# Optimization experiments

Hardware: AMD Instinct MI355X
Metric: run time of the kernel (lower is better)

The kernel has to match this reference:

```python
import jax, jax.numpy as jnp
import numpy as np

GROUP_SIZE = 256
QMIN_W, QMAX_W = -8, 7  # int4
QMIN_A, QMAX_A = -128, 127  # int8


def per_token_fake_quant(x):
    """torchao choose_qparams_per_token_asymmetric + quant + dequant (int8)."""
    mn = jnp.minimum(jnp.min(x, axis=-1, keepdims=True), 0.0)
    mx = jnp.maximum(jnp.max(x, axis=-1, keepdims=True), 0.0)
    eps = jnp.finfo(jnp.float32).eps
    scale = jnp.maximum((mx - mn) / float(QMAX_A - QMIN_A), eps)
    dmin = mn / scale
    dmax = mx / scale
    zp = jnp.where((QMIN_A + dmin) + (QMAX_A + dmax) > 0, QMIN_A - dmin, QMAX_A - dmax)
    zp = jnp.round(jnp.clip(zp, QMIN_A, QMAX_A))
    q = jnp.clip(jnp.round(x / scale) + zp, QMIN_A, QMAX_A)
    return (q - zp) * scale


def setup_inputs() -> dict:
    key = jax.random.key(0)
    k1, k2, k3, k4 = jax.random.split(key, 4)
    T, O, I = 8192, 4096, 4096
    x = jax.random.normal(k1, (T, I), dtype=jnp.float32)
    weight = jax.random.randint(k2, (O, I), QMIN_W, QMAX_W + 1, dtype=jnp.int32)
    scales = jax.random.uniform(k3, (O, I // GROUP_SIZE), dtype=jnp.float32,
                                minval=0.005, maxval=0.02)
    zeros = jnp.round(jax.random.uniform(k4, (O, I // GROUP_SIZE), dtype=jnp.float32,
                                         minval=-4.0, maxval=4.0))
    return {"x": x, "weight": weight, "scales": scales, "zeros": zeros}


def reference(x, weight, scales, zeros):
    # dynamic per-token int8 fake-quant of the activation
    x_dq = per_token_fake_quant(x.astype(jnp.float32))
    # groupwise int4 weight dequant: (w - zero) * scale per group
    O, I = weight.shape
    w = weight.astype(jnp.float32).reshape(O, I // GROUP_SIZE, GROUP_SIZE)
    w_dq = ((w - zeros[..., None]) * scales[..., None]).reshape(O, I)
    # linear: [T, I] @ [I, O] -> [T, O]
    return jnp.einsum('ti,oi->to', x_dq, w_dq)
```

## Files before the change

kernel.cpp:

```cpp
#include <hip/hip_runtime.h>
#include <hip/hip_bf16.h>
#include <math.h>

typedef __attribute__((ext_vector_type(8))) __bf16 bf16x8;
typedef __attribute__((ext_vector_type(4))) float f32x4;

#define BM 256
#define BN 256
#define BK 64

__device__ __forceinline__ void glds16(const void* g, void* l) {
  __builtin_amdgcn_global_load_lds(
      (const __attribute__((address_space(1))) void*)g,
      (__attribute__((address_space(3))) void*)l, 16, 0, 0);
}

__device__ __forceinline__ unsigned short f2bf(float f) {
  __hip_bfloat16 h = __float2bfloat16(f);
  return __builtin_bit_cast(unsigned short, h);
}

__global__ __launch_bounds__(256) void prep_x(const float* __restrict__ x,
                                              ushort* __restrict__ xq,
                                              int I) {
  const int wave = threadIdx.x >> 6, lane = threadIdx.x & 63;
  const int row = blockIdx.x * 4 + wave;
  const float4* xr = (const float4*)(x + (size_t)row * I);
  float4 v[16];
#pragma unroll
  for (int j = 0; j < 16; ++j) v[j] = xr[lane + j * 64];
  float mn = 0.f, mx = 0.f;
#pragma unroll
  for (int j = 0; j < 16; ++j) {
    mn = fminf(mn, fminf(fminf(v[j].x, v[j].y), fminf(v[j].z, v[j].w)));
    mx = fmaxf(mx, fmaxf(fmaxf(v[j].x, v[j].y), fmaxf(v[j].z, v[j].w)));
  }
#pragma unroll
  for (int off = 32; off > 0; off >>= 1) {
    mn = fminf(mn, __shfl_xor(mn, off));
    mx = fmaxf(mx, __shfl_xor(mx, off));
  }
  const float scale = fmaxf((mx - mn) / 255.0f, 1.1920928955078125e-07f);
  const float dmin = mn / scale, dmax = mx / scale;
  float zp = ((-128.0f + dmin) + (127.0f + dmax) > 0.0f) ? (-128.0f - dmin)
                                                         : (127.0f - dmax);
  zp = rintf(fminf(fmaxf(zp, -128.0f), 127.0f));
  const float rs = 1.0f / scale;
  ushort4* xo = (ushort4*)(xq + (size_t)row * I);
#pragma unroll
  for (int j = 0; j < 16; ++j) {
    ushort4 o;
    float q;
    q = fminf(fmaxf(rintf(v[j].x * rs) + zp, -128.f), 127.f);
    o.x = f2bf((q - zp) * scale);
    q = fminf(fmaxf(rintf(v[j].y * rs) + zp, -128.f), 127.f);
    o.y = f2bf((q - zp) * scale);
    q = fminf(fmaxf(rintf(v[j].z * rs) + zp, -128.f), 127.f);
    o.z = f2bf((q - zp) * scale);
    q = fminf(fmaxf(rintf(v[j].w * rs) + zp, -128.f), 127.f);
    o.w = f2bf((q - zp) * scale);
    xo[lane + j * 64] = o;
  }
}

__global__ __launch_bounds__(256) void prep_w(const int* __restrict__ w,
                                              const float* __restrict__ scales,
                                              const float* __restrict__ zeros,
                                              ushort* __restrict__ wq) {
  const long long base = (long long)blockIdx.x * 2048 + threadIdx.x;
  const int4* wr = (const int4*)w;
  ushort4* wo = (ushort4*)wq;
  int4 wv[8];
#pragma unroll
  for (int it = 0; it < 8; ++it) wv[it] = wr[base + (size_t)it * 256];
#pragma unroll
  for (int it = 0; it < 8; ++it) {
    const long long c = base + (size_t)it * 256;
    const int g = __builtin_amdgcn_readfirstlane((int)(c >> 6));
    const float s = scales[g];
    const float z = zeros[g];
    ushort4 ov;
    ov.x = f2bf(((float)wv[it].x - z) * s);
    ov.y = f2bf(((float)wv[it].y - z) * s);
    ov.z = f2bf(((float)wv[it].z - z) * s);
    ov.w = f2bf(((float)wv[it].w - z) * s);
    wo[c] = ov;
  }
}

__global__ __launch_bounds__(512, 2) void gemm_bt256(
    const ushort* __restrict__ A, const ushort* __restrict__ B,
    float* __restrict__ C, int M, int N, int K) {
  __shared__ __align__(16) ushort As[2][BM * BK];
  __shared__ __align__(16) ushort Bs[2][BN * BK];
  const int tid = threadIdx.x;
  const int wave = tid >> 6, lane = tid & 63;
  const int wm = wave >> 2;
  const int wn = wave & 3;

  const int nwg = gridDim.x;
  const int bid = blockIdx.x;
  const int swz =
      ((nwg & 7) == 0) ? ((bid & 7) * (nwg >> 3) + (bid >> 3)) : bid;
  const int ntn = N / BN;
  const int by = swz / ntn, bx = swz % ntn;
  const int bm0 = by * BM, bn0 = bx * BN;

  const int ldr = lane >> 3;
  const int ldc = ((lane & 7) ^ ldr) * 8;
  const ushort* Ag = A + (size_t)(bm0 + wave * 16 + ldr) * K + ldc;
  const ushort* Bg = B + (size_t)(bn0 + wave * 16 + ldr) * K + ldc;

#define STAGE_A(b, h, kt)                                        \
  do {                                                           \
    glds16(Ag + (size_t)((h) * 128) * K + (size_t)(kt) * BK,     \
           &As[b][((h) * 128 + wave * 16) * BK]);                \
    glds16(Ag + (size_t)((h) * 128 + 8) * K + (size_t)(kt) * BK, \
           &As[b][((h) * 128 + wave * 16 + 8) * BK]);            \
  } while (0)
#define STAGE_B(b, h, kt)                                        \
  do {                                                           \
    glds16(Bg + (size_t)((h) * 128) * K + (size_t)(kt) * BK,     \
           &Bs[b][((h) * 128 + wave * 16) * BK]);                \
    glds16(Bg + (size_t)((h) * 128 + 8) * K + (size_t)(kt) * BK, \
           &Bs[b][((h) * 128 + wave * 16 + 8) * BK]);            \
  } while (0)

  const int mrow = lane & 15;
  const int kc = lane >> 4;
  const int sw = mrow & 7;
  const int c0 = (kc ^ sw) * 8;
  const int c1 = ((4 + kc) ^ sw) * 8;
  const int aBase = (wm * 128 + mrow) * BK;
  const int bBase = (wn * 64 + mrow) * BK;

  f32x4 acc[8][4];
#pragma unroll
  for (int i = 0; i < 8; ++i)
#pragma unroll
    for (int j = 0; j < 4; ++j) acc[i][j] = (f32x4){0.f, 0.f, 0.f, 0.f};

  const int NT = K / BK;

  STAGE_A(0, 0, 0);
  STAGE_A(0, 1, 0);
  STAGE_B(0, 0, 0);
  STAGE_B(0, 1, 0);
  STAGE_B(1, 0, 1);
  STAGE_B(1, 1, 1);
  asm volatile("s_waitcnt vmcnt(4)" ::: "memory");
  __builtin_amdgcn_sched_barrier(0);
  __builtin_amdgcn_s_barrier();

  bf16x8 a[4][2], b[4][2];

#define MFMA8(MI0, NI0)                                                    \
  __builtin_amdgcn_s_setprio(1);                                           \
  _Pragma("unroll") for (int ks = 0; ks < 2; ++ks)                         \
      _Pragma("unroll") for (int mi = 0; mi < 4; ++mi)                     \
          _Pragma("unroll") for (int ni = 0; ni < 2; ++ni) acc[(MI0) + mi] \
              [(NI0) + ni] = __builtin_amdgcn_mfma_f32_16x16x32_bf16(      \
                  a[mi][ks], b[(NI0) + ni][ks], acc[(MI0) + mi][(NI0) + ni], \
                  0, 0, 0);                                                \
  __builtin_amdgcn_s_setprio(0);

#define KTILE(CUR, KT, DO_SA, DO_SB, WAIT4)                          \
  do {                                                               \
    const ushort* Ac = As[CUR];                                      \
    const ushort* Bc = Bs[CUR];                                      \
                             \
    _Pragma("unroll") for (int mi = 0; mi < 4; ++mi) {               \
      a[mi][0] = *(const bf16x8*)&Ac[aBase + mi * (16 * BK) + c0];   \
      a[mi][1] = *(const bf16x8*)&Ac[aBase + mi * (16 * BK) + c1];   \
    }                                                                \
    _Pragma("unroll") for (int ni = 0; ni < 2; ++ni) {               \
      b[ni][0] = *(const bf16x8*)&Bc[bBase + ni * (16 * BK) + c0];   \
      b[ni][1] = *(const bf16x8*)&Bc[bBase + ni * (16 * BK) + c1];   \
    }                                                                \
    if (DO_SA) STAGE_A(1 - (CUR), 0, (KT) + 1);                      \
    __builtin_amdgcn_s_barrier();                                    \
    MFMA8(0, 0)                                                      \
    __builtin_amdgcn_s_barrier();                                    \
                             \
    _Pragma("unroll") for (int ni = 2; ni < 4; ++ni) {               \
      b[ni][0] = *(const bf16x8*)&Bc[bBase + ni * (16 * BK) + c0];   \
      b[ni][1] = *(const bf16x8*)&Bc[bBase + ni * (16 * BK) + c1];   \
    }                                                                \
    if (DO_SA) STAGE_A(1 - (CUR), 1, (KT) + 1);                      \
    __builtin_amdgcn_s_barrier();                                    \
    MFMA8(0, 2)                                                      \
    __builtin_amdgcn_s_barrier();                                    \
                             \
    _Pragma("unroll") for (int mi = 0; mi < 4; ++mi) {               \
      a[mi][0] =                                                     \
          *(const bf16x8*)&Ac[aBase + (mi + 4) * (16 * BK) + c0];    \
      a[mi][1] =                                                     \
          *(const bf16x8*)&Ac[aBase + (mi + 4) * (16 * BK) + c1];    \
    }                                                                \
    if (DO_SB) STAGE_B(CUR, 0, (KT) + 2);                            \
    __builtin_amdgcn_s_barrier();                                    \
    MFMA8(4, 2)                                                      \
    __builtin_amdgcn_s_barrier();                                    \
                             \
    if (DO_SB) STAGE_B(CUR, 1, (KT) + 2);                            \
    if (WAIT4)                                                       \
      asm volatile("s_waitcnt vmcnt(4)" ::: "memory");               \
    else                                                             \
      asm volatile("s_waitcnt vmcnt(0)" ::: "memory");               \
    __builtin_amdgcn_sched_barrier(0);                               \
    __builtin_amdgcn_s_barrier();                                    \
    MFMA8(4, 0)                                                      \
    __builtin_amdgcn_s_barrier();                                    \
  } while (0)

  int kt = 0;
  for (; kt < NT - 2; kt += 2) {
    KTILE(0, kt, 1, 1, 1);
    KTILE(1, kt + 1, 1, 1, 1);
  }
  KTILE(0, kt, 1, 0, 0);
  KTILE(1, kt + 1, 0, 0, 0);

  const int col = lane & 15;
  const int rq = (lane >> 4) * 4;
#pragma unroll
  for (int mi = 0; mi < 8; ++mi)
#pragma unroll
    for (int ni = 0; ni < 4; ++ni) {
      const int r0 = bm0 + wm * 128 + mi * 16 + rq;
      const int c = bn0 + wn * 64 + ni * 16 + col;
#pragma unroll
      for (int r = 0; r < 4; ++r)
        C[(size_t)(r0 + r) * N + c] = acc[mi][ni][r];
    }
#undef KTILE
#undef MFMA8
#undef STAGE_A
#undef STAGE_B
}

extern "C" void kernel_launch(void* const* d_in, const int* in_sizes, int n_in,
                              void* d_out, int out_size, void* d_ws,
                              size_t ws_size, hipStream_t stream) {
  const float* x = (const float*)d_in[0];
  const int* w = (const int*)d_in[1];
  const float* scales = (const float*)d_in[2];
  const float* zeros = (const float*)d_in[3];
  float* out = (float*)d_out;

  const double ii =
      sqrt((double)in_sizes[0] * (double)in_sizes[1] / (double)out_size);
  const int I = (int)(ii + 0.5);
  const int T = in_sizes[0] / I;
  const int O = in_sizes[1] / I;

  ushort* xq = (ushort*)d_ws;
  ushort* wq = xq + (size_t)T * I;

  prep_x<<<T / 4, 256, 0, stream>>>(x, xq, I);
  prep_w<<<(int)(((long long)O * I) >> 13), 256, 0, stream>>>(w, scales,
                                                              zeros, wq);
  gemm_bt256<<<(O / BN) * (T / BM), 512, 0, stream>>>(xq, wq, out, T, O, I);
}
```

Before: 506.9 us.

## Replace bf16 GEMM with int8 MFMA and fold group scales and zero points

Activations and weights are now stored as exact int8 values: the per-token quantized x, and the weight with its group zero subtracted. The GEMM uses i32 int8 MFMA over 128-byte K tiles and applies each tile's per-group weight scale to the integer partial sums in fp32. The activation zero point is removed in the epilogue using a precomputed per-output-row sum U of scaled weights, plus the per-token scale and zero. This halves operand bytes and uses the higher-rate int8 matrix path, but adds VALU work converting and scaling integer partials on every K tile, and more LDS for the scale table.

```diff
diff --git a/kernel.cpp b/kernel.cpp
--- a/kernel.cpp
+++ b/kernel.cpp
@@ -2,12 +2,12 @@
 #include <hip/hip_bf16.h>
 #include <math.h>
 
-typedef __attribute__((ext_vector_type(8))) __bf16 bf16x8;
+typedef __attribute__((ext_vector_type(4))) int i32x4;
 typedef __attribute__((ext_vector_type(4))) float f32x4;
 
 #define BM 256
 #define BN 256
-#define BK 64
+#define BKB 128
 
 __device__ __forceinline__ void glds16(const void* g, void* l) {
   __builtin_amdgcn_global_load_lds(
@@ -15,13 +15,10 @@
       (__attribute__((address_space(3))) void*)l, 16, 0, 0);
 }
 
-__device__ __forceinline__ unsigned short f2bf(float f) {
-  __hip_bfloat16 h = __float2bfloat16(f);
-  return __builtin_bit_cast(unsigned short, h);
-}
-
 __global__ __launch_bounds__(256) void prep_x(const float* __restrict__ x,
-                                              ushort* __restrict__ xq,
+                                              char* __restrict__ xq,
+                                              float* __restrict__ sct,
+                                              float* __restrict__ zpt,
                                               int I) {
   const int wave = threadIdx.x >> 6, lane = threadIdx.x & 63;
   const int row = blockIdx.x * 4 + wave;
@@ -46,30 +43,33 @@
                                                          : (127.0f - dmax);
   zp = rintf(fminf(fmaxf(zp, -128.0f), 127.0f));
   const float rs = 1.0f / scale;
-  ushort4* xo = (ushort4*)(xq + (size_t)row * I);
+  if (lane == 0) {
+    sct[row] = scale;
+    zpt[row] = zp;
+  }
+  int* xo = (int*)(xq + (size_t)row * I);
 #pragma unroll
   for (int j = 0; j < 16; ++j) {
-    ushort4 o;
-    float q;
-    q = fminf(fmaxf(rintf(v[j].x * rs) + zp, -128.f), 127.f);
-    o.x = f2bf((q - zp) * scale);
-    q = fminf(fmaxf(rintf(v[j].y * rs) + zp, -128.f), 127.f);
-    o.y = f2bf((q - zp) * scale);
-    q = fminf(fmaxf(rintf(v[j].z * rs) + zp, -128.f), 127.f);
-    o.z = f2bf((q - zp) * scale);
-    q = fminf(fmaxf(rintf(v[j].w * rs) + zp, -128.f), 127.f);
-    o.w = f2bf((q - zp) * scale);
-    xo[lane + j * 64] = o;
+    const float q0 = fminf(fmaxf(rintf(v[j].x * rs) + zp, -128.f), 127.f);
+    const float q1 = fminf(fmaxf(rintf(v[j].y * rs) + zp, -128.f), 127.f);
+    const float q2 = fminf(fmaxf(rintf(v[j].z * rs) + zp, -128.f), 127.f);
+    const float q3 = fminf(fmaxf(rintf(v[j].w * rs) + zp, -128.f), 127.f);
+    xo[lane + j * 64] = ((int)q0 & 255) | (((int)q1 & 255) << 8) |
+                        (((int)q2 & 255) << 16) | ((int)q3 << 24);
   }
 }
 
 __global__ __launch_bounds__(256) void prep_w(const int* __restrict__ w,
                                               const float* __restrict__ scales,
                                               const float* __restrict__ zeros,
-                                              ushort* __restrict__ wq) {
-  const long long base = (long long)blockIdx.x * 2048 + threadIdx.x;
+                                              char* __restrict__ wq,
+                                              float* __restrict__ U) {
+  __shared__ float sg[32];
+  const int tid = threadIdx.x;
+  const int wave = tid >> 6, lane = tid & 63;
+  const long long base = (long long)blockIdx.x * 2048 + tid;
   const int4* wr = (const int4*)w;
-  ushort4* wo = (ushort4*)wq;
+  int* wo = (int*)wq;
   int4 wv[8];
 #pragma unroll
   for (int it = 0; it < 8; ++it) wv[it] = wr[base + (size_t)it * 256];
@@ -78,21 +78,32 @@
     const long long c = base + (size_t)it * 256;
     const int g = __builtin_amdgcn_readfirstlane((int)(c >> 6));
     const float s = scales[g];
-    const float z = zeros[g];
-    ushort4 ov;
-    ov.x = f2bf(((float)wv[it].x - z) * s);
-    ov.y = f2bf(((float)wv[it].y - z) * s);
-    ov.z = f2bf(((float)wv[it].z - z) * s);
-    ov.w = f2bf(((float)wv[it].w - z) * s);
-    wo[c] = ov;
-  }
-}
-
-__global__ __launch_bounds__(512, 2) void gemm_bt256(
-    const ushort* __restrict__ A, const ushort* __restrict__ B,
-    float* __restrict__ C, int M, int N, int K) {
-  __shared__ __align__(16) ushort As[2][BM * BK];
-  __shared__ __align__(16) ushort Bs[2][BN * BK];
+    const int zi = (int)zeros[g];
+    const int a0 = wv[it].x - zi, a1 = wv[it].y - zi;
+    const int a2 = wv[it].z - zi, a3 = wv[it].w - zi;
+    wo[c] = (a0 & 255) | ((a1 & 255) << 8) | ((a2 & 255) << 16) | (a3 << 24);
+    int cs = a0 + a1 + a2 + a3;
+#pragma unroll
+    for (int off = 32; off > 0; off >>= 1) cs += __shfl_xor(cs, off);
+    if (lane == 0) sg[wave + it * 4] = s * (float)cs;
+  }
+  __syncthreads();
+  if (tid < 2) {
+    float u = 0.f;
+#pragma unroll
+    for (int k = 0; k < 16; ++k) u += sg[tid * 16 + k];
+    U[blockIdx.x * 2 + tid] = u;
+  }
+}
+
+__global__ __launch_bounds__(512, 2) void gemm_i8(
+    const char* __restrict__ A, const char* __restrict__ B,
+    const float* __restrict__ scales, const float* __restrict__ sct,
+    const float* __restrict__ zpt, const float* __restrict__ U,
+    float* __restrict__ C, int N, int K, int G) {
+  __shared__ __align__(16) char As[2][BM * BKB];
+  __shared__ __align__(16) char Bs[2][BN * BKB];
+  __shared__ __align__(16) float scl[BN * 16];
   const int tid = threadIdx.x;
   const int wave = tid >> 6, lane = tid & 63;
   const int wm = wave >> 2;
@@ -107,32 +118,40 @@
   const int bm0 = by * BM, bn0 = bx * BN;
 
   const int ldr = lane >> 3;
-  const int ldc = ((lane & 7) ^ ldr) * 8;
-  const ushort* Ag = A + (size_t)(bm0 + wave * 16 + ldr) * K + ldc;
-  const ushort* Bg = B + (size_t)(bn0 + wave * 16 + ldr) * K + ldc;
-
-#define STAGE_A(b, h, kt)                                        \
-  do {                                                           \
-    glds16(Ag + (size_t)((h) * 128) * K + (size_t)(kt) * BK,     \
-           &As[b][((h) * 128 + wave * 16) * BK]);                \
-    glds16(Ag + (size_t)((h) * 128 + 8) * K + (size_t)(kt) * BK, \
-           &As[b][((h) * 128 + wave * 16 + 8) * BK]);            \
+  const int ldc = ((lane & 7) ^ ldr) * 16;
+  const char* Ag = A + (size_t)(bm0 + wave * 16 + ldr) * K + ldc;
+  const char* Bg = B + (size_t)(bn0 + wave * 16 + ldr) * K + ldc;
+
+#define STAGE_A(b_, h, kt)                                        \
+  do {                                                            \
+    glds16(Ag + (size_t)((h) * 128) * K + (size_t)(kt) * BKB,     \
+           &As[b_][((h) * 128 + wave * 16) * BKB]);               \
+    glds16(Ag + (size_t)((h) * 128 + 8) * K + (size_t)(kt) * BKB, \
+           &As[b_][((h) * 128 + wave * 16 + 8) * BKB]);           \
   } while (0)
-#define STAGE_B(b, h, kt)                                        \
-  do {                                                           \
-    glds16(Bg + (size_t)((h) * 128) * K + (size_t)(kt) * BK,     \
-           &Bs[b][((h) * 128 + wave * 16) * BK]);                \
-    glds16(Bg + (size_t)((h) * 128 + 8) * K + (size_t)(kt) * BK, \
-           &Bs[b][((h) * 128 + wave * 16 + 8) * BK]);            \
+#define STAGE_B(b_, h, kt)                                        \
+  do {                                                            \
+    glds16(Bg + (size_t)((h) * 128) * K + (size_t)(kt) * BKB,     \
+           &Bs[b_][((h) * 128 + wave * 16) * BKB]);               \
+    glds16(Bg + (size_t)((h) * 128 + 8) * K + (size_t)(kt) * BKB, \
+           &Bs[b_][((h) * 128 + wave * 16 + 8) * BKB]);           \
   } while (0)
 
   const int mrow = lane & 15;
   const int kc = lane >> 4;
   const int sw = mrow & 7;
-  const int c0 = (kc ^ sw) * 8;
-  const int c1 = ((4 + kc) ^ sw) * 8;
-  const int aBase = (wm * 128 + mrow) * BK;
-  const int bBase = (wn * 64 + mrow) * BK;
+  const int c0 = ((kc) ^ sw) * 16;
+  const int c1 = ((4 + kc) ^ sw) * 16;
+  const int aBase = (wm * 128 + mrow) * BKB;
+  const int bBase = (wn * 64 + mrow) * BKB;
+  const int col = lane & 15;
+
+  {
+    const float4* sp = (const float4*)(scales + (size_t)bn0 * G);
+    float4* sd = (float4*)scl;
+    sd[tid] = sp[tid];
+    sd[tid + 512] = sp[tid + 512];
+  }
 
   f32x4 acc[8][4];
 #pragma unroll
@@ -140,7 +159,7 @@
 #pragma unroll
     for (int j = 0; j < 4; ++j) acc[i][j] = (f32x4){0.f, 0.f, 0.f, 0.f};
 
-  const int NT = K / BK;
+  const int NT = K / BKB;
 
   STAGE_A(0, 0, 0);
   STAGE_A(0, 1, 0);
@@ -149,68 +168,84 @@
   STAGE_B(1, 0, 1);
   STAGE_B(1, 1, 1);
   asm volatile("s_waitcnt vmcnt(4)" ::: "memory");
+  asm volatile("s_waitcnt lgkmcnt(0)" ::: "memory");
   __builtin_amdgcn_sched_barrier(0);
   __builtin_amdgcn_s_barrier();
 
-  bf16x8 a[4][2], b[4][2];
-
-#define MFMA8(MI0, NI0)                                                    \
-  __builtin_amdgcn_s_setprio(1);                                           \
-  _Pragma("unroll") for (int ks = 0; ks < 2; ++ks)                         \
-      _Pragma("unroll") for (int mi = 0; mi < 4; ++mi)                     \
-          _Pragma("unroll") for (int ni = 0; ni < 2; ++ni) acc[(MI0) + mi] \
-              [(NI0) + ni] = __builtin_amdgcn_mfma_f32_16x16x32_bf16(      \
-                  a[mi][ks], b[(NI0) + ni][ks], acc[(MI0) + mi][(NI0) + ni], \
-                  0, 0, 0);                                                \
+  i32x4 a[4][2], b[4][2], qd[4][2];
+  float ssv[4];
+
+#define MMQ(NI0)                                                          \
+  __builtin_amdgcn_s_setprio(1);                                          \
+  _Pragma("unroll") for (int mi = 0; mi < 4; ++mi)                        \
+      _Pragma("unroll") for (int nj = 0; nj < 2; ++nj) {                  \
+    i32x4 t0 = __builtin_amdgcn_mfma_i32_16x16x64_i8(                     \
+        a[mi][0], b[(NI0) + nj][0], (i32x4){0, 0, 0, 0}, 0, 0, 0);        \
+    qd[mi][nj] = __builtin_amdgcn_mfma_i32_16x16x64_i8(                   \
+        a[mi][1], b[(NI0) + nj][1], t0, 0, 0, 0);                         \
+  }                                                                       \
   __builtin_amdgcn_s_setprio(0);
 
-#define KTILE(CUR, KT, DO_SA, DO_SB, WAIT4)                          \
-  do {                                                               \
-    const ushort* Ac = As[CUR];                                      \
-    const ushort* Bc = Bs[CUR];                                      \
-                             \
-    _Pragma("unroll") for (int mi = 0; mi < 4; ++mi) {               \
-      a[mi][0] = *(const bf16x8*)&Ac[aBase + mi * (16 * BK) + c0];   \
-      a[mi][1] = *(const bf16x8*)&Ac[aBase + mi * (16 * BK) + c1];   \
-    }                                                                \
-    _Pragma("unroll") for (int ni = 0; ni < 2; ++ni) {               \
-      b[ni][0] = *(const bf16x8*)&Bc[bBase + ni * (16 * BK) + c0];   \
-      b[ni][1] = *(const bf16x8*)&Bc[bBase + ni * (16 * BK) + c1];   \
-    }                                                                \
-    if (DO_SA) STAGE_A(1 - (CUR), 0, (KT) + 1);                      \
-    __builtin_amdgcn_s_barrier();                                    \
-    MFMA8(0, 0)                                                      \
-    __builtin_amdgcn_s_barrier();                                    \
-                             \
-    _Pragma("unroll") for (int ni = 2; ni < 4; ++ni) {               \
-      b[ni][0] = *(const bf16x8*)&Bc[bBase + ni * (16 * BK) + c0];   \
-      b[ni][1] = *(const bf16x8*)&Bc[bBase + ni * (16 * BK) + c1];   \
-    }                                                                \
-    if (DO_SA) STAGE_A(1 - (CUR), 1, (KT) + 1);                      \
-    __builtin_amdgcn_s_barrier();                                    \
-    MFMA8(0, 2)                                                      \
-    __builtin_amdgcn_s_barrier();                                    \
-                             \
-    _Pragma("unroll") for (int mi = 0; mi < 4; ++mi) {               \
-      a[mi][0] =                                                     \
-          *(const bf16x8*)&Ac[aBase + (mi + 4) * (16 * BK) + c0];    \
-      a[mi][1] =                                                     \
-          *(const bf16x8*)&Ac[aBase + (mi + 4) * (16 * BK) + c1];    \
-    }                                                                \
-    if (DO_SB) STAGE_B(CUR, 0, (KT) + 2);                            \
-    __builtin_amdgcn_s_barrier();                                    \
-    MFMA8(4, 2)                                                      \
-    __builtin_amdgcn_s_barrier();                                    \
-                             \
-    if (DO_SB) STAGE_B(CUR, 1, (KT) + 2);                            \
-    if (WAIT4)                                                       \
-      asm volatile("s_waitcnt vmcnt(4)" ::: "memory");               \
-    else                                                             \
-      asm volatile("s_waitcnt vmcnt(0)" ::: "memory");               \
-    __builtin_amdgcn_sched_barrier(0);                               \
-    __builtin_amdgcn_s_barrier();                                    \
-    MFMA8(4, 0)                                                      \
-    __builtin_amdgcn_s_barrier();                                    \
+#define FOLD(MI0, NI0)                                                 \
+  _Pragma("unroll") for (int mi = 0; mi < 4; ++mi)                     \
+      _Pragma("unroll") for (int nj = 0; nj < 2; ++nj) {               \
+    const float sv = ssv[(NI0) + nj];                                  \
+    _Pragma("unroll") for (int r = 0; r < 4; ++r)                      \
+        acc[(MI0) + mi][(NI0) + nj][r] += sv * (float)qd[mi][nj][r];   \
+  }
+
+#define LDB2(NI0, GK)                                                       \
+  _Pragma("unroll") for (int nj = 0; nj < 2; ++nj) {                        \
+    b[(NI0) + nj][0] =                                                      \
+        *(const i32x4*)&Bc[bBase + ((NI0) + nj) * (16 * BKB) + c0];         \
+    b[(NI0) + nj][1] =                                                      \
+        *(const i32x4*)&Bc[bBase + ((NI0) + nj) * (16 * BKB) + c1];         \
+    ssv[(NI0) + nj] = scl[(wn * 64 + ((NI0) + nj) * 16 + col) * 16 + (GK)]; \
+  }
+#define LDA(MI0)                                                           \
+  _Pragma("unroll") for (int mi = 0; mi < 4; ++mi) {                       \
+    a[mi][0] = *(const i32x4*)&Ac[aBase + ((MI0) + mi) * (16 * BKB) + c0]; \
+    a[mi][1] = *(const i32x4*)&Ac[aBase + ((MI0) + mi) * (16 * BKB) + c1]; \
+  }
+
+#define KTILE(CUR, KT, DO_SA, DO_SB, WAIT4)            \
+  do {                                                 \
+    const char* Ac = As[CUR];                          \
+    const char* Bc = Bs[CUR];                          \
+    const int gk = (KT) >> 1;                          \
+                         \
+    LDA(0)                                             \
+    LDB2(0, gk)                                        \
+    if (DO_SA) STAGE_A(1 - (CUR), 0, (KT) + 1);        \
+    __builtin_amdgcn_s_barrier();                      \
+    MMQ(0)                                             \
+    FOLD(0, 0)                                         \
+    __builtin_amdgcn_s_barrier();                      \
+                         \
+    LDB2(2, gk)                                        \
+    if (DO_SA) STAGE_A(1 - (CUR), 1, (KT) + 1);        \
+    __builtin_amdgcn_s_barrier();                      \
+    MMQ(2)                                             \
+    FOLD(0, 2)                                         \
+    __builtin_amdgcn_s_barrier();                      \
+     \
+    LDA(4)                                             \
+    if (DO_SB) STAGE_B(CUR, 0, (KT) + 2);              \
+    __builtin_amdgcn_s_barrier();                      \
+    MMQ(2)                                             \
+    FOLD(4, 2)                                         \
+    __builtin_amdgcn_s_barrier();                      \
+     \
+    if (DO_SB) STAGE_B(CUR, 1, (KT) + 2);              \
+    if (WAIT4)                                         \
+      asm volatile("s_waitcnt vmcnt(4)" ::: "memory"); \
+    else                                               \
+      asm volatile("s_waitcnt vmcnt(0)" ::: "memory"); \
+    __builtin_amdgcn_sched_barrier(0);                 \
+    __builtin_amdgcn_s_barrier();                      \
+    MMQ(0)                                             \
+    FOLD(4, 0)                                         \
+    __builtin_amdgcn_s_barrier();                      \
   } while (0)
 
   int kt = 0;
@@ -221,20 +256,29 @@
   KTILE(0, kt, 1, 0, 0);
   KTILE(1, kt + 1, 0, 0, 0);
 
-  const int col = lane & 15;
   const int rq = (lane >> 4) * 4;
-#pragma unroll
-  for (int mi = 0; mi < 8; ++mi)
-#pragma unroll
-    for (int ni = 0; ni < 4; ++ni) {
-      const int r0 = bm0 + wm * 128 + mi * 16 + rq;
-      const int c = bn0 + wn * 64 + ni * 16 + col;
-#pragma unroll
-      for (int r = 0; r < 4; ++r)
-        C[(size_t)(r0 + r) * N + c] = acc[mi][ni][r];
+  float un[4];
+#pragma unroll
+  for (int ni = 0; ni < 4; ++ni) un[ni] = U[bn0 + wn * 64 + ni * 16 + col];
+#pragma unroll
+  for (int mi = 0; mi < 8; ++mi) {
+    const int r0 = bm0 + wm * 128 + mi * 16 + rq;
+#pragma unroll
+    for (int r = 0; r < 4; ++r) {
+      const float sc = sct[r0 + r];
+      const float zp = zpt[r0 + r];
+#pragma unroll
+      for (int ni = 0; ni < 4; ++ni) {
+        const int c = bn0 + wn * 64 + ni * 16 + col;
+        C[(size_t)(r0 + r) * N + c] = sc * (acc[mi][ni][r] - zp * un[ni]);
+      }
     }
+  }
 #undef KTILE
-#undef MFMA8
+#undef LDA
+#undef LDB2
+#undef FOLD
+#undef MMQ
 #undef STAGE_A
 #undef STAGE_B
 }
@@ -253,12 +297,17 @@
   const int I = (int)(ii + 0.5);
   const int T = in_sizes[0] / I;
   const int O = in_sizes[1] / I;
-
-  ushort* xq = (ushort*)d_ws;
-  ushort* wq = xq + (size_t)T * I;
-
-  prep_x<<<T / 4, 256, 0, stream>>>(x, xq, I);
+  const int G = I / 256;
+
+  char* xqi = (char*)d_ws;
+  char* wqi = xqi + (size_t)T * I;
+  float* sct = (float*)(wqi + (size_t)O * I);
+  float* zpt = sct + T;
+  float* U = zpt + T;
+
+  prep_x<<<T / 4, 256, 0, stream>>>(x, xqi, sct, zpt, I);
   prep_w<<<(int)(((long long)O * I) >> 13), 256, 0, stream>>>(w, scales,
-                                                              zeros, wq);
-  gemm_bt256<<<(O / BN) * (T / BM), 512, 0, stream>>>(xq, wq, out, T, O, I);
-}
+                                                              zeros, wqi, U);
+  gemm_i8<<<(O / BN) * (T / BM), 512, 0, stream>>>(xqi, wqi, scales, sct, zpt,
+                                                   U, out, O, I, G);
+}
```

Result: slower. 1.352 ms (+166.7%).
